# Optimization experiments

Measured on AMD Instinct MI355X. Metric: run time of the kernel, lower is better.

Reference implementation:

```python
import jax, jax.numpy as jnp
import numpy as np

S, B, E, H, M = 1024, 4, 1024, 16, 128  # seq, batch, embed, heads, model_dims (key width)
V = E // H                              # value_dims = 64
_WSCALE = 1.0 / np.sqrt(E)              # keep softmax logits O(1)


def _cplx(re, im):
    return jax.lax.complex(re, im)


def setup_inputs() -> dict:
    key = jax.random.key(0)
    ks = jax.random.split(key, 10)
    n = lambda k, shp: jax.random.normal(k, shp, dtype=jnp.float32)
    w = lambda k, shp: n(k, shp) * np.float32(_WSCALE / np.sqrt(2.0))
    return {
        "logits_re": n(ks[0], (S, B, E)),
        "logits_im": n(ks[1], (S, B, E)),
        "wq_re": w(ks[2], (H, M, E)), "wq_im": w(ks[3], (H, M, E)),
        "wk_re": w(ks[4], (H, M, E)), "wk_im": w(ks[5], (H, M, E)),
        "wv_re": w(ks[6], (H, V, E)), "wv_im": w(ks[7], (H, V, E)),
        "wo_re": w(ks[8], (E, E)),    "wo_im": w(ks[9], (E, E)),
    }


def reference(logits_re, logits_im, wq_re, wq_im, wk_re, wk_im,
              wv_re, wv_im, wo_re, wo_im):
    x = _cplx(logits_re, logits_im)          # (s, b, e) complex64
    wq = _cplx(wq_re, wq_im)                 # (h, m, e)
    wk = _cplx(wk_re, wk_im)
    wv = _cplx(wv_re, wv_im)                 # (h, v, e)
    wo = _cplx(wo_re, wo_im)                 # (e, e)

    q = jnp.einsum('hme,sbe->bhsm', wq, x)   # (b, h, s, m)
    k = jnp.einsum('hme,sbe->bhsm', wk, x)
    v = jnp.einsum('hve,sbe->bhsv', wv, x)   # (b, h, s, v)

    scores = jnp.einsum('bhsm,bhtm->bhst', q, k)         # complex, no conjugation (matches torch matmul)
    amp = jnp.abs(scores)                                # -> float32
    causal = jnp.triu(jnp.ones((S, S), dtype=bool), 1)   # True above diagonal -> masked
    amp = jnp.where(causal, -jnp.inf, amp) / jnp.sqrt(jnp.float32(M))
    attn = jax.nn.softmax(amp, axis=-1).astype(scores.dtype)  # cast back to complex64

    upd = jnp.einsum('bhst,bhtv->bhsv', attn, v)         # (b, h, s, v)
    upd = upd.transpose(2, 0, 1, 3).reshape(S, B, E)     # 's2 b (h v)'
    out = jnp.einsum('sbe,ef->sbf', upd, wo) + x         # residual
    # complex output returned as stacked (real, imag) float32 for harness compatibility
    return jnp.stack([out.real, out.imag])
```

## Files before the change

### kernel.cpp

```cpp
#include <hip/hip_runtime.h>
#include <math.h>

#define S_DIM 1024
#define B_DIM 4
#define E_DIM 1024
#define H_DIM 16
#define M_DIM 128
#define V_DIM 64

typedef __attribute__((ext_vector_type(8))) short short8;
typedef __attribute__((ext_vector_type(4))) float f32x4;
typedef __attribute__((ext_vector_type(4))) int int4v;

__device__ __forceinline__ unsigned short f2bf(float f) {
    union { float f; unsigned u; } v; v.f = f;
    unsigned r = v.u + 0x7FFFu + ((v.u >> 16) & 1u);
    return (unsigned short)(r >> 16);
}

__device__ __forceinline__ void async16(const unsigned short* g, unsigned short* l) {
    __builtin_amdgcn_global_load_lds(
        (const __attribute__((address_space(1))) void*)g,
        (__attribute__((address_space(3))) void*)l,
        16, 0, 0);
}

__global__ __launch_bounds__(256) void convert_pair(
    const float* __restrict__ re, const float* __restrict__ im,
    unsigned short* __restrict__ dre, unsigned short* __restrict__ dim_, int n4)
{
    int i = blockIdx.x * 256 + threadIdx.x;
    if (i >= n4) return;
    float4 r = ((const float4*)re)[i];
    float4 m = ((const float4*)im)[i];
    ushort4 ro, mo;
    ro.x = f2bf(r.x); ro.y = f2bf(r.y); ro.z = f2bf(r.z); ro.w = f2bf(r.w);
    mo.x = f2bf(m.x); mo.y = f2bf(m.y); mo.z = f2bf(m.z); mo.w = f2bf(m.w);
    ((ushort4*)dre)[i] = ro;
    ((ushort4*)dim_)[i] = mo;
}

__global__ __launch_bounds__(256) void transpose_wo(
    const float* __restrict__ wore, const float* __restrict__ woim,
    unsigned short* __restrict__ wtre, unsigned short* __restrict__ wtim)
{
    __shared__ float tr[32][33], ti[32][33];
    const int bx = blockIdx.x * 32;
    const int by = blockIdx.y * 32;
    const int tx = threadIdx.x & 31, ty = threadIdx.x >> 5;
    for (int i = ty; i < 32; i += 8) {
        tr[i][tx] = wore[(bx + i) * E_DIM + by + tx];
        ti[i][tx] = woim[(bx + i) * E_DIM + by + tx];
    }
    __syncthreads();
    for (int i = ty; i < 32; i += 8) {
        wtre[(by + i) * E_DIM + bx + tx] = f2bf(tr[tx][i]);
        wtim[(by + i) * E_DIM + bx + tx] = f2bf(ti[tx][i]);
    }
}

__global__ __launch_bounds__(256) void vtrans(
    const unsigned short* __restrict__ vrp, const unsigned short* __restrict__ vip,
    unsigned short* __restrict__ vrt, unsigned short* __restrict__ vit)
{
    __shared__ unsigned short tl[2][64][66];
    const int tid = threadIdx.x;
    const int t0 = blockIdx.x * 64;
    const int bh = blockIdx.y;
    #pragma unroll
    for (int pl = 0; pl < 2; ++pl) {
        const unsigned short* src = pl ? vip : vrp;
        #pragma unroll
        for (int p = 0; p < 2; ++p) {
            const int row = p * 32 + (tid >> 3);
            const int col = (tid & 7) * 8;
            short8 d = *(const short8*)&src[((size_t)bh * S_DIM + t0 + row) * V_DIM + col];
            #pragma unroll
            for (int j = 0; j < 8; ++j) tl[pl][row][col + j] = (unsigned short)d[j];
        }
    }
    __syncthreads();
    #pragma unroll
    for (int pl = 0; pl < 2; ++pl) {
        unsigned short* dst = pl ? vit : vrt;
        #pragma unroll
        for (int p = 0; p < 2; ++p) {
            const int v = p * 32 + (tid >> 3);
            const int tc = (tid & 7) * 8;
            short8 d;
            #pragma unroll
            for (int j = 0; j < 8; ++j) d[j] = (short)tl[pl][tc + j][v];
            *(short8*)&dst[((size_t)bh * V_DIM + v) * S_DIM + t0 + tc] = d;
        }
    }
}

template<int MODE>
__global__ __launch_bounds__(256, 3) void cgemm(
    const unsigned short* __restrict__ Are, const unsigned short* __restrict__ Aim,
    const unsigned short* __restrict__ Bre, const unsigned short* __restrict__ Bim,
    unsigned short* __restrict__ qrp, unsigned short* __restrict__ qip,
    unsigned short* __restrict__ krp, unsigned short* __restrict__ kip,
    unsigned short* __restrict__ vrp, unsigned short* __restrict__ vip,
    const float* __restrict__ xre, const float* __restrict__ xim,
    float* __restrict__ out)
{
    __shared__ __align__(16) unsigned short lds[24576];
    const int tid  = threadIdx.x;
    const int wave = tid >> 6;
    const int lane = tid & 63;
    const int r0 = blockIdx.x * 128;
    const int j0 = blockIdx.y * 64;
    const int wm = (wave >> 1) * 64;
    const int wn = (wave & 1) * 32;

    f32x4 accre[4][2], accim[4][2];
    #pragma unroll
    for (int i = 0; i < 4; ++i)
        #pragma unroll
        for (int j = 0; j < 2; ++j) {
            accre[i][j] = (f32x4){0.f, 0.f, 0.f, 0.f};
            accim[i][j] = (f32x4){0.f, 0.f, 0.f, 0.f};
        }

    const int srow = lane >> 2;
    const int scol = ((lane & 3) ^ ((lane >> 3) & 3)) * 8;

    const int fr = lane & 15;
    const int xc = ((lane >> 4) ^ ((lane >> 1) & 3)) * 8;

    #define STAGE(sl, bb) { \
        const int kg = (sl) * 32; \
        unsigned short* b_ = &lds[(bb) * 12288]; \
        _Pragma("unroll") \
        for (int c = 0; c < 2; ++c) { \
            const int row0 = wave * 32 + c * 16; \
            const size_t g = (size_t)(r0 + row0 + srow) * E_DIM + kg + scol; \
            async16(Are + g, b_ + row0 * 32); \
            async16(Aim + g, b_ + 4096 + row0 * 32); \
        } \
        { \
            const int row0 = wave * 16; \
            const size_t g = (size_t)(j0 + row0 + srow) * E_DIM + kg + scol; \
            async16(Bre + g, b_ + 8192 + row0 * 32); \
            async16(Bim + g, b_ + 10240 + row0 * 32); \
        } }

    STAGE(0, 0)
    asm volatile("s_waitcnt vmcnt(0)" ::: "memory");
    __builtin_amdgcn_s_barrier();

    #pragma unroll 1
    for (int s = 0; s < 32; ++s) {
        if (s < 31) STAGE(s + 1, (s + 1) & 1)

        const unsigned short* buf = &lds[(s & 1) * 12288];
        short8 ar[4], ai[4], brr[2], bii[2];
        #pragma unroll
        for (int im = 0; im < 4; ++im) {
            const int ro = (wm + im * 16 + fr) * 32 + xc;
            ar[im] = *(const short8*)&buf[ro];
            ai[im] = *(const short8*)&buf[4096 + ro];
        }
        #pragma unroll
        for (int jn = 0; jn < 2; ++jn) {
            const int ro = (wn + jn * 16 + fr) * 32 + xc;
            brr[jn] = *(const short8*)&buf[8192 + ro];
            bii[jn] = *(const short8*)&buf[10240 + ro];
        }
        asm volatile("s_waitcnt lgkmcnt(0)" ::: "memory");
        __builtin_amdgcn_sched_barrier(0);

        __builtin_amdgcn_s_setprio(1);
        #pragma unroll
        for (int jn = 0; jn < 2; ++jn) {
            int4v t = *(int4v*)&bii[jn];
            t = t ^ (int)0x80008000;
            const short8 bin = *(short8*)&t;
            #pragma unroll
            for (int im = 0; im < 4; ++im) {
                accre[im][jn] = __builtin_amdgcn_mfma_f32_16x16x32_bf16(ar[im], brr[jn], accre[im][jn], 0, 0, 0);
                accre[im][jn] = __builtin_amdgcn_mfma_f32_16x16x32_bf16(ai[im], bin,     accre[im][jn], 0, 0, 0);
                accim[im][jn] = __builtin_amdgcn_mfma_f32_16x16x32_bf16(ar[im], bii[jn], accim[im][jn], 0, 0, 0);
                accim[im][jn] = __builtin_amdgcn_mfma_f32_16x16x32_bf16(ai[im], brr[jn], accim[im][jn], 0, 0, 0);
            }
        }
        __builtin_amdgcn_s_setprio(0);

        if (s < 31) {
            asm volatile("s_waitcnt vmcnt(0)" ::: "memory");
            __builtin_amdgcn_s_barrier();
        }
    }
    #undef STAGE

    #pragma unroll
    for (int im = 0; im < 4; ++im) {
        #pragma unroll
        for (int reg = 0; reg < 4; ++reg) {
            const int r = r0 + wm + im * 16 + (lane >> 4) * 4 + reg;
            #pragma unroll
            for (int jn = 0; jn < 2; ++jn) {
                const int j = j0 + wn + jn * 16 + fr;
                const float vr = accre[im][jn][reg];
                const float vi = accim[im][jn][reg];
                if (MODE == 0) {
                    const int s = r >> 2, b = r & 3;
                    if (j < 2048) {
                        const int h = j >> 7, m = j & 127;
                        const size_t off = ((size_t)(b * H_DIM + h) * S_DIM + s) * M_DIM + m;
                        qrp[off] = f2bf(vr); qip[off] = f2bf(vi);
                    } else if (j < 4096) {
                        const int jl = j - 2048, h = jl >> 7, m = jl & 127;
                        const size_t off = ((size_t)(b * H_DIM + h) * S_DIM + s) * M_DIM + m;
                        krp[off] = f2bf(vr); kip[off] = f2bf(vi);
                    } else {
                        const int jl = j - 4096, h = jl >> 6, vv = jl & 63;
                        const size_t off = ((size_t)(b * H_DIM + h) * S_DIM + s) * V_DIM + vv;
                        vrp[off] = f2bf(vr); vip[off] = f2bf(vi);
                    }
                } else {
                    const int idx = r * E_DIM + j;
                    out[idx] = vr + xre[idx];
                    out[S_DIM * B_DIM * E_DIM + idx] = vi + xim[idx];
                }
            }
        }
    }
}

__global__ __launch_bounds__(256, 2) void attn_mfma(
    const unsigned short* __restrict__ qr, const unsigned short* __restrict__ qi,
    const unsigned short* __restrict__ kr, const unsigned short* __restrict__ ki,
    const unsigned short* __restrict__ vrt, const unsigned short* __restrict__ vit,
    unsigned short* __restrict__ updre, unsigned short* __restrict__ updim)
{
    __shared__ __align__(16) unsigned short Ks[2][64][136];
    __shared__ __align__(16) unsigned short Vs[2][64][72];
    __shared__ __align__(16) unsigned short Ps[4][16][80];

    const int tid  = threadIdx.x;
    const int wave = tid >> 6;
    const int lane = tid & 63;
    const int qt = (int)gridDim.x - 1 - blockIdx.x;
    const int bh = blockIdx.y;
    const int q0 = qt * 64;
    const size_t base_qk = (size_t)bh * S_DIM * M_DIM;
    const size_t base_v  = (size_t)bh * V_DIM * S_DIM;

    const int fr = lane & 15;
    const int fg = lane >> 4;
    const int fk = fg * 8;

    const int krow = tid >> 4, kcol = (tid & 15) * 8;
    const int vrow = tid >> 3, vcol = (tid & 7) * 8;

    #pragma unroll
    for (int pl = 0; pl < 2; ++pl) {
        const unsigned short* src = pl ? qi : qr;
        #pragma unroll
        for (int p = 0; p < 4; ++p)
            *(short8*)&Ks[pl][p * 16 + krow][kcol] =
                *(const short8*)&src[base_qk + (size_t)(q0 + p * 16 + krow) * M_DIM + kcol];
    }
    __syncthreads();
    short8 Bqr[4], Bqi[4];
    {
        const int qrow = wave * 16 + fr;
        #pragma unroll
        for (int ks = 0; ks < 4; ++ks) {
            Bqr[ks] = *(const short8*)&Ks[0][qrow][ks * 32 + fk];
            Bqi[ks] = *(const short8*)&Ks[1][qrow][ks * 32 + fk];
        }
    }

    f32x4 Ore[4], Oim[4];
    #pragma unroll
    for (int vt = 0; vt < 4; ++vt) {
        Ore[vt] = (f32x4){0.f, 0.f, 0.f, 0.f};
        Oim[vt] = (f32x4){0.f, 0.f, 0.f, 0.f};
    }
    float mrun = -INFINITY, lrun = 0.f;

    const float scale = 0.088388347648318447f;
    const int qglob = q0 + wave * 16 + fr;

    short8 pk[2][4], pv[2][2];
    #pragma unroll
    for (int pl = 0; pl < 2; ++pl) {
        const unsigned short* src = pl ? ki : kr;
        #pragma unroll
        for (int p = 0; p < 4; ++p)
            pk[pl][p] = *(const short8*)&src[base_qk + (size_t)(p * 16 + krow) * M_DIM + kcol];
    }
    #pragma unroll
    for (int pl = 0; pl < 2; ++pl) {
        const unsigned short* src = pl ? vit : vrt;
        #pragma unroll
        for (int p = 0; p < 2; ++p)
            pv[pl][p] = *(const short8*)&src[base_v + (size_t)(p * 32 + vrow) * S_DIM + vcol];
    }

    for (int t0 = 0; t0 <= q0; t0 += 64) {
        __syncthreads();
        #pragma unroll
        for (int pl = 0; pl < 2; ++pl) {
            #pragma unroll
            for (int p = 0; p < 4; ++p)
                *(short8*)&Ks[pl][p * 16 + krow][kcol] = pk[pl][p];
            #pragma unroll
            for (int p = 0; p < 2; ++p)
                *(short8*)&Vs[pl][p * 32 + vrow][vcol] = pv[pl][p];
        }
        __syncthreads();

        if (t0 + 64 <= q0) {
            const int tn = t0 + 64;
            #pragma unroll
            for (int pl = 0; pl < 2; ++pl) {
                const unsigned short* src = pl ? ki : kr;
                #pragma unroll
                for (int p = 0; p < 4; ++p)
                    pk[pl][p] = *(const short8*)&src[base_qk + (size_t)(tn + p * 16 + krow) * M_DIM + kcol];
            }
            #pragma unroll
            for (int pl = 0; pl < 2; ++pl) {
                const unsigned short* src = pl ? vit : vrt;
                #pragma unroll
                for (int p = 0; p < 2; ++p)
                    pv[pl][p] = *(const short8*)&src[base_v + (size_t)(p * 32 + vrow) * S_DIM + tn + vcol];
            }
        }

        f32x4 Sre[4], Sim[4];
        #pragma unroll
        for (int tt = 0; tt < 4; ++tt) {
            Sre[tt] = (f32x4){0.f, 0.f, 0.f, 0.f};
            Sim[tt] = (f32x4){0.f, 0.f, 0.f, 0.f};
            const int trow = tt * 16 + fr;
            #pragma unroll
            for (int ks = 0; ks < 4; ++ks) {
                const short8 Akr = *(const short8*)&Ks[0][trow][ks * 32 + fk];
                const short8 Aki = *(const short8*)&Ks[1][trow][ks * 32 + fk];
                int4v t = *(int4v*)&Aki;
                t = t ^ (int)0x80008000;
                const short8 Akin = *(short8*)&t;
                Sre[tt] = __builtin_amdgcn_mfma_f32_16x16x32_bf16(Akr,  Bqr[ks], Sre[tt], 0, 0, 0);
                Sre[tt] = __builtin_amdgcn_mfma_f32_16x16x32_bf16(Akin, Bqi[ks], Sre[tt], 0, 0, 0);
                Sim[tt] = __builtin_amdgcn_mfma_f32_16x16x32_bf16(Akr,  Bqi[ks], Sim[tt], 0, 0, 0);
                Sim[tt] = __builtin_amdgcn_mfma_f32_16x16x32_bf16(Aki,  Bqr[ks], Sim[tt], 0, 0, 0);
            }
        }

        float amp[4][4];
        float rowmax = -INFINITY;
        #pragma unroll
        for (int tt = 0; tt < 4; ++tt) {
            #pragma unroll
            for (int r = 0; r < 4; ++r) {
                const int tg = t0 + tt * 16 + fg * 4 + r;
                const float re = Sre[tt][r], im = Sim[tt][r];
                const float a = sqrtf(re * re + im * im) * scale;
                const float av = (tg > qglob) ? -INFINITY : a;
                amp[tt][r] = av;
                rowmax = fmaxf(rowmax, av);
            }
        }
        rowmax = fmaxf(rowmax, __shfl_xor(rowmax, 16));
        rowmax = fmaxf(rowmax, __shfl_xor(rowmax, 32));
        const float nm = fmaxf(mrun, rowmax);
        const float alpha = __expf(mrun - nm);
        mrun = nm;
        float psum = 0.f;
        #pragma unroll
        for (int tt = 0; tt < 4; ++tt) {
            #pragma unroll
            for (int r = 0; r < 4; ++r) {
                const float p = __expf(amp[tt][r] - nm);
                psum += p;
                Ps[wave][fr][tt * 16 + fg * 4 + r] = f2bf(p);
            }
        }
        psum += __shfl_xor(psum, 16);
        psum += __shfl_xor(psum, 32);
        lrun = lrun * alpha + psum;

        #pragma unroll
        for (int vt = 0; vt < 4; ++vt)
            #pragma unroll
            for (int r = 0; r < 4; ++r) { Ore[vt][r] *= alpha; Oim[vt][r] *= alpha; }

        const short8 Bp0 = *(const short8*)&Ps[wave][fr][fk];
        const short8 Bp1 = *(const short8*)&Ps[wave][fr][32 + fk];
        #pragma unroll
        for (int vt = 0; vt < 4; ++vt) {
            const int vr2 = vt * 16 + fr;
            const short8 Ar0 = *(const short8*)&Vs[0][vr2][fk];
            const short8 Ar1 = *(const short8*)&Vs[0][vr2][32 + fk];
            const short8 Ai0 = *(const short8*)&Vs[1][vr2][fk];
            const short8 Ai1 = *(const short8*)&Vs[1][vr2][32 + fk];
            Ore[vt] = __builtin_amdgcn_mfma_f32_16x16x32_bf16(Ar0, Bp0, Ore[vt], 0, 0, 0);
            Ore[vt] = __builtin_amdgcn_mfma_f32_16x16x32_bf16(Ar1, Bp1, Ore[vt], 0, 0, 0);
            Oim[vt] = __builtin_amdgcn_mfma_f32_16x16x32_bf16(Ai0, Bp0, Oim[vt], 0, 0, 0);
            Oim[vt] = __builtin_amdgcn_mfma_f32_16x16x32_bf16(Ai1, Bp1, Oim[vt], 0, 0, 0);
        }
    }

    const int b = bh >> 4, h = bh & 15;
    const float inv = 1.0f / lrun;
    const size_t base = ((size_t)(qglob * B_DIM + b)) * E_DIM + h * V_DIM;
    #pragma unroll
    for (int vt = 0; vt < 4; ++vt) {
        ushort4 pr, pi;
        pr.x = f2bf(Ore[vt][0] * inv); pr.y = f2bf(Ore[vt][1] * inv);
        pr.z = f2bf(Ore[vt][2] * inv); pr.w = f2bf(Ore[vt][3] * inv);
        pi.x = f2bf(Oim[vt][0] * inv); pi.y = f2bf(Oim[vt][1] * inv);
        pi.z = f2bf(Oim[vt][2] * inv); pi.w = f2bf(Oim[vt][3] * inv);
        *(ushort4*)&updre[base + vt * 16 + fg * 4] = pr;
        *(ushort4*)&updim[base + vt * 16 + fg * 4] = pi;
    }
}

extern "C" void kernel_launch(void* const* d_in, const int* in_sizes, int n_in,
                              void* d_out, int out_size, void* d_ws, size_t ws_size,
                              hipStream_t stream) {
    const float* xre  = (const float*)d_in[0];
    const float* xim  = (const float*)d_in[1];
    const float* wqre = (const float*)d_in[2];
    const float* wqim = (const float*)d_in[3];
    const float* wkre = (const float*)d_in[4];
    const float* wkim = (const float*)d_in[5];
    const float* wvre = (const float*)d_in[6];
    const float* wvim = (const float*)d_in[7];
    const float* wore = (const float*)d_in[8];
    const float* woim = (const float*)d_in[9];
    float* out = (float*)d_out;

    char* p = (char*)d_ws;
    const size_t QK = (size_t)B_DIM * H_DIM * S_DIM * M_DIM;
    const size_t VS = (size_t)B_DIM * H_DIM * S_DIM * V_DIM;
    const size_t SBE = (size_t)S_DIM * B_DIM * E_DIM;
    unsigned short* qrw = (unsigned short*)p;  p += QK * 2;
    unsigned short* qiw = (unsigned short*)p;  p += QK * 2;
    unsigned short* krw = (unsigned short*)p;  p += QK * 2;
    unsigned short* kiw = (unsigned short*)p;  p += QK * 2;
    unsigned short* vrw = (unsigned short*)p;  p += VS * 2;
    unsigned short* viw = (unsigned short*)p;  p += VS * 2;
    unsigned short* vrt = (unsigned short*)p;  p += VS * 2;
    unsigned short* vit = (unsigned short*)p;  p += VS * 2;
    unsigned short* updre = (unsigned short*)p; p += SBE * 2;
    unsigned short* updim = (unsigned short*)p; p += SBE * 2;
    unsigned short* xbre  = (unsigned short*)p; p += SBE * 2;
    unsigned short* xbim  = (unsigned short*)p; p += SBE * 2;
    unsigned short* wbre  = (unsigned short*)p; p += (size_t)5120 * E_DIM * 2;
    unsigned short* wbim  = (unsigned short*)p; p += (size_t)5120 * E_DIM * 2;
    unsigned short* wtre  = (unsigned short*)p; p += (size_t)E_DIM * E_DIM * 2;
    unsigned short* wtim  = (unsigned short*)p; p += (size_t)E_DIM * E_DIM * 2;

    convert_pair<<<4096, 256, 0, stream>>>(xre, xim, xbre, xbim, 1048576);
    convert_pair<<<2048, 256, 0, stream>>>(wqre, wqim, wbre, wbim, 524288);
    convert_pair<<<2048, 256, 0, stream>>>(wkre, wkim, wbre + 2048*1024, wbim + 2048*1024, 524288);
    convert_pair<<<1024, 256, 0, stream>>>(wvre, wvim, wbre + 4096*1024, wbim + 4096*1024, 262144);
    transpose_wo<<<dim3(32, 32), 256, 0, stream>>>(wore, woim, wtre, wtim);

    cgemm<0><<<dim3(32, 80), 256, 0, stream>>>(xbre, xbim, wbre, wbim,
                                               qrw, qiw, krw, kiw, vrw, viw,
                                               nullptr, nullptr, nullptr);
    vtrans<<<dim3(16, 64), 256, 0, stream>>>(vrw, viw, vrt, vit);
    attn_mfma<<<dim3(16, 64), 256, 0, stream>>>(qrw, qiw, krw, kiw, vrt, vit, updre, updim);
    cgemm<1><<<dim3(32, 16), 256, 0, stream>>>(updre, updim, wtre, wtim,
                                               nullptr, nullptr, nullptr, nullptr, nullptr, nullptr,
                                               xre, xim, out);
}
```

Measured before the change: 501.2 us.

## Merge conversion launches, swap GEMM grid order, move setprio to attention MFMAs

Combines four fp32-to-bf16 conversion launches into one kernel that picks its source by thread index, cutting launch overhead. Swaps the cgemm grid axes so consecutive blocks walk the weight (column) dimension and share A-row tiles in cache. Drops the explicit lgkmcnt wait, sched_barrier and setprio in the GEMM inner loop. Adds setprio around the MFMA blocks in the attention kernel instead. These are several independent scheduling tweaks whose effects may offset one another.

```diff
diff --git a/kernel.cpp b/kernel.cpp
--- a/kernel.cpp
+++ b/kernel.cpp
@@ -25,19 +25,29 @@
         16, 0, 0);
 }
 
-__global__ __launch_bounds__(256) void convert_pair(
-    const float* __restrict__ re, const float* __restrict__ im,
-    unsigned short* __restrict__ dre, unsigned short* __restrict__ dim_, int n4)
+__global__ __launch_bounds__(256) void convert_all(
+    const float* __restrict__ xre,  const float* __restrict__ xim,
+    const float* __restrict__ wqre, const float* __restrict__ wqim,
+    const float* __restrict__ wkre, const float* __restrict__ wkim,
+    const float* __restrict__ wvre, const float* __restrict__ wvim,
+    unsigned short* __restrict__ xbre, unsigned short* __restrict__ xbim,
+    unsigned short* __restrict__ wbre, unsigned short* __restrict__ wbim)
 {
-    int i = blockIdx.x * 256 + threadIdx.x;
-    if (i >= n4) return;
-    float4 r = ((const float4*)re)[i];
-    float4 m = ((const float4*)im)[i];
+    const int i = blockIdx.x * 256 + threadIdx.x;
+    const float *re, *im;
+    unsigned short *dr, *di;
+    int j;
+    if (i < 1048576)      { re = xre;  im = xim;  dr = xbre;               di = xbim;               j = i; }
+    else if (i < 1572864) { re = wqre; im = wqim; dr = wbre;               di = wbim;               j = i - 1048576; }
+    else if (i < 2097152) { re = wkre; im = wkim; dr = wbre + 2048 * 1024; di = wbim + 2048 * 1024; j = i - 1572864; }
+    else                  { re = wvre; im = wvim; dr = wbre + 4096 * 1024; di = wbim + 4096 * 1024; j = i - 2097152; }
+    float4 r = ((const float4*)re)[j];
+    float4 m = ((const float4*)im)[j];
     ushort4 ro, mo;
     ro.x = f2bf(r.x); ro.y = f2bf(r.y); ro.z = f2bf(r.z); ro.w = f2bf(r.w);
     mo.x = f2bf(m.x); mo.y = f2bf(m.y); mo.z = f2bf(m.z); mo.w = f2bf(m.w);
-    ((ushort4*)dre)[i] = ro;
-    ((ushort4*)dim_)[i] = mo;
+    ((ushort4*)dr)[j] = ro;
+    ((ushort4*)di)[j] = mo;
 }
 
 __global__ __launch_bounds__(256) void transpose_wo(
@@ -109,8 +119,8 @@
     const int tid  = threadIdx.x;
     const int wave = tid >> 6;
     const int lane = tid & 63;
-    const int r0 = blockIdx.x * 128;
-    const int j0 = blockIdx.y * 64;
+    const int r0 = blockIdx.y * 128;
+    const int j0 = blockIdx.x * 64;
     const int wm = (wave >> 1) * 64;
     const int wn = (wave & 1) * 32;
 
@@ -168,10 +178,7 @@
             brr[jn] = *(const short8*)&buf[8192 + ro];
             bii[jn] = *(const short8*)&buf[10240 + ro];
         }
-        asm volatile("s_waitcnt lgkmcnt(0)" ::: "memory");
-        __builtin_amdgcn_sched_barrier(0);
-
-        __builtin_amdgcn_s_setprio(1);
+
         #pragma unroll
         for (int jn = 0; jn < 2; ++jn) {
             int4v t = *(int4v*)&bii[jn];
@@ -185,7 +192,6 @@
                 accim[im][jn] = __builtin_amdgcn_mfma_f32_16x16x32_bf16(ai[im], brr[jn], accim[im][jn], 0, 0, 0);
             }
         }
-        __builtin_amdgcn_s_setprio(0);
 
         if (s < 31) {
             asm volatile("s_waitcnt vmcnt(0)" ::: "memory");
@@ -333,6 +339,7 @@
         }
 
         f32x4 Sre[4], Sim[4];
+        __builtin_amdgcn_s_setprio(1);
         #pragma unroll
         for (int tt = 0; tt < 4; ++tt) {
             Sre[tt] = (f32x4){0.f, 0.f, 0.f, 0.f};
@@ -351,6 +358,7 @@
                 Sim[tt] = __builtin_amdgcn_mfma_f32_16x16x32_bf16(Aki,  Bqr[ks], Sim[tt], 0, 0, 0);
             }
         }
+        __builtin_amdgcn_s_setprio(0);
 
         float amp[4][4];
         float rowmax = -INFINITY;
@@ -392,6 +400,7 @@
 
         const short8 Bp0 = *(const short8*)&Ps[wave][fr][fk];
         const short8 Bp1 = *(const short8*)&Ps[wave][fr][32 + fk];
+        __builtin_amdgcn_s_setprio(1);
         #pragma unroll
         for (int vt = 0; vt < 4; ++vt) {
             const int vr2 = vt * 16 + fr;
@@ -404,6 +413,7 @@
             Oim[vt] = __builtin_amdgcn_mfma_f32_16x16x32_bf16(Ai0, Bp0, Oim[vt], 0, 0, 0);
             Oim[vt] = __builtin_amdgcn_mfma_f32_16x16x32_bf16(Ai1, Bp1, Oim[vt], 0, 0, 0);
         }
+        __builtin_amdgcn_s_setprio(0);
     }
 
     const int b = bh >> 4, h = bh & 15;
@@ -457,18 +467,16 @@
     unsigned short* wtre  = (unsigned short*)p; p += (size_t)E_DIM * E_DIM * 2;
     unsigned short* wtim  = (unsigned short*)p; p += (size_t)E_DIM * E_DIM * 2;
 
-    convert_pair<<<4096, 256, 0, stream>>>(xre, xim, xbre, xbim, 1048576);
-    convert_pair<<<2048, 256, 0, stream>>>(wqre, wqim, wbre, wbim, 524288);
-    convert_pair<<<2048, 256, 0, stream>>>(wkre, wkim, wbre + 2048*1024, wbim + 2048*1024, 524288);
-    convert_pair<<<1024, 256, 0, stream>>>(wvre, wvim, wbre + 4096*1024, wbim + 4096*1024, 262144);
+    convert_all<<<9216, 256, 0, stream>>>(xre, xim, wqre, wqim, wkre, wkim, wvre, wvim,
+                                          xbre, xbim, wbre, wbim);
     transpose_wo<<<dim3(32, 32), 256, 0, stream>>>(wore, woim, wtre, wtim);
 
-    cgemm<0><<<dim3(32, 80), 256, 0, stream>>>(xbre, xbim, wbre, wbim,
+    cgemm<0><<<dim3(80, 32), 256, 0, stream>>>(xbre, xbim, wbre, wbim,
                                                qrw, qiw, krw, kiw, vrw, viw,
                                                nullptr, nullptr, nullptr);
     vtrans<<<dim3(16, 64), 256, 0, stream>>>(vrw, viw, vrt, vit);
     attn_mfma<<<dim3(16, 64), 256, 0, stream>>>(qrw, qiw, krw, kiw, vrt, vit, updre, updim);
-    cgemm<1><<<dim3(32, 16), 256, 0, stream>>>(updre, updim, wtre, wtim,
+    cgemm<1><<<dim3(16, 32), 256, 0, stream>>>(updre, updim, wtre, wtim,
                                                nullptr, nullptr, nullptr, nullptr, nullptr, nullptr,
                                                xre, xim, out);
 }
```

New measurement: 476.4 us. -5.0%, faster.
